# Kernel optimization log

Measured on AMD Instinct MI355X. Metric: run time of the kernel, lower is better.

## Reference

```python
import jax, jax.numpy as jnp
import numpy as np

EPS = 1e-5          # nn.LayerNorm default eps
THRESH = 0.4        # min_entity_score
K = 20              # max_entities_per_text
NUM_TYPES = 8       # len(EntityType) (not in source; fixed constant)


def _mlp(x, w1, b1, g, be, w2, b2):
    """Linear -> LayerNorm -> GELU(exact) -> (Dropout=eval identity) -> Linear."""
    h = x @ w1 + b1
    mu = h.mean(-1, keepdims=True)
    var = ((h - mu) ** 2).mean(-1, keepdims=True)
    h = (h - mu) * jax.lax.rsqrt(var + EPS) * g + be
    h = jax.nn.gelu(h, approximate=False)
    return h @ w2 + b2


def setup_inputs() -> dict:
    key = jax.random.key(0)
    ks = jax.random.split(key, 10)
    B, S, D, H, T = 8, 4096, 1024, 256, NUM_TYPES

    def lin(k, i, o):
        s = 1.0 / np.sqrt(i)
        return jax.random.uniform(k, (i, o), jnp.float32, -s, s)

    return {
        "hidden_states": jax.random.normal(ks[0], (B, S, D), jnp.float32),
        "attention_mask": jax.random.randint(ks[1], (B, S), 0, 2).astype(jnp.int32),
        # entity_scorer params
        "sc_w1": lin(ks[2], D, H), "sc_b1": jnp.zeros((H,), jnp.float32),
        "sc_g": jnp.ones((H,), jnp.float32), "sc_be": jnp.zeros((H,), jnp.float32),
        "sc_w2": lin(ks[3], H, 1), "sc_b2": jnp.zeros((1,), jnp.float32),
        # span_enhancer params
        "en_w1": lin(ks[4], D, H), "en_b1": jnp.zeros((H,), jnp.float32),
        "en_g": jnp.ones((H,), jnp.float32), "en_be": jnp.zeros((H,), jnp.float32),
        "en_w2": lin(ks[5], H, D), "en_b2": jnp.zeros((D,), jnp.float32),
        # type_classifier params
        "ty_w1": lin(ks[6], D, H), "ty_b1": jnp.zeros((H,), jnp.float32),
        "ty_g": jnp.ones((H,), jnp.float32), "ty_be": jnp.zeros((H,), jnp.float32),
        "ty_w2": lin(ks[7], H, T), "ty_b2": jnp.zeros((T,), jnp.float32),
    }


def reference(hidden_states, attention_mask,
              sc_w1, sc_b1, sc_g, sc_be, sc_w2, sc_b2,
              en_w1, en_b1, en_g, en_be, en_w2, en_b2,
              ty_w1, ty_b1, ty_g, ty_be, ty_w2, ty_b2):
    B, S, D = hidden_states.shape
    # per-token entity scores [B, S]
    scores = jax.nn.sigmoid(_mlp(hidden_states, sc_w1, sc_b1, sc_g, sc_be, sc_w2, sc_b2))[..., 0]
    scores = scores * attention_mask.astype(scores.dtype)
    # parallel run-length encoding of spans (replaces serial python loop):
    # a token is inside a span iff score >= thresh and unmasked; spans break on
    # below-threshold or masked tokens, exactly as the serial RLE does.
    above = (scores >= THRESH) & (attention_mask > 0)
    prev = jnp.pad(above[:, :-1], ((0, 0), (1, 0)))
    start = above & ~prev
    sid = jnp.clip(jnp.cumsum(start.astype(jnp.int32), axis=1) - 1, 0)  # span label per token
    seg = (sid + jnp.arange(B, dtype=jnp.int32)[:, None] * S).reshape(-1)
    w = above.astype(scores.dtype)
    nseg = B * S
    span_len = jax.ops.segment_sum(w.reshape(-1), seg, num_segments=nseg).reshape(B, S)
    span_sum = jax.ops.segment_sum((scores * w).reshape(-1), seg, num_segments=nseg).reshape(B, S)
    rep_sum = jax.ops.segment_sum((hidden_states * w[..., None]).reshape(B * S, D), seg,
                                  num_segments=nseg).reshape(B, S, D)
    denom = jnp.maximum(span_len, 1.0)
    avg = span_sum / denom                      # mean token score per span
    valid = (span_len > 0) & (avg >= THRESH)    # avg-score threshold from original
    sel = jnp.where(valid, avg, -1.0)
    # keep at most K highest-scoring spans per batch row (matches global sort + per-batch cap)
    top_vals, top_idx = jax.lax.top_k(sel, K)   # [B, K]
    valid_k = (top_vals >= THRESH).astype(scores.dtype)
    reps = jnp.take_along_axis(rep_sum, top_idx[..., None], axis=1)
    lens = jnp.take_along_axis(denom, top_idx, axis=1)
    reps = reps / lens[..., None] * valid_k[..., None]      # span mean-pooled hidden states
    enhanced = _mlp(reps, en_w1, en_b1, en_g, en_be, en_w2, en_b2) * valid_k[..., None]
    type_logits = _mlp(enhanced, ty_w1, ty_b1, ty_g, ty_be, ty_w2, ty_b2)
    type_probs = jax.nn.softmax(type_logits, axis=-1)
    entity_types = jnp.argmax(type_logits, axis=-1)
    entity_scores = top_vals * valid_k
    return scores, enhanced, type_logits, entity_scores, type_probs, entity_types, valid_k
```

## Files before the change

kernel.cpp:

```cpp
#include <hip/hip_runtime.h>
#include <hip/hip_bf16.h>

#define S_LEN 4096
#define BATCH 8
#define DMODEL 1024
#define HDIM 256
#define NTYPES 8
#define KMAX 20
#define NSLOT (BATCH*KMAX)
#define THRESH 0.4f
#define LN_EPS 1e-5f
#define RSQRT2 0.70710678118654752f

#define O_SCORES 0
#define O_ENH    32768
#define O_TLOG   196608
#define O_ESC    197888
#define O_TPROB  198048
#define O_TYPE   199328
#define O_VALIDK 199488

#define WS_SCORES   0
#define WS_SPSTART  32768
#define WS_SPLEN    49152
#define WS_SPAVG    65536
#define WS_NSP      81920
#define WS_SELSTART 81936
#define WS_SELLEN   82096
#define WS_SELAVG   82256
#define WS_SELVALID 82416
#define WS_IMG      82576

typedef _Float16 f16x8 __attribute__((ext_vector_type(8)));
typedef float f32x16 __attribute__((ext_vector_type(16)));

__device__ __forceinline__ float gelu_exact(float v) {
    return 0.5f * v * (1.0f + erff(v * RSQRT2));
}
__device__ __forceinline__ int kkey(int r) { return (r ^ (r >> 2)) & 3; }

#define GLL16(g, l) __builtin_amdgcn_global_load_lds( \
    (const __attribute__((address_space(1))) unsigned int*)(g), \
    (__attribute__((address_space(3))) unsigned int*)(l), 16, 0, 0)

__global__ __launch_bounds__(256) void k_prep(
    const float* __restrict__ W1, _Float16* __restrict__ IMG)
{
    const int c = blockIdx.x;
    const int n = threadIdx.x;
#pragma unroll
    for (int j = 0; j < 4; j++) {
        f16x8 hv, lv;
#pragma unroll
        for (int e = 0; e < 8; e++) {
            float w = W1[(size_t)(c * 32 + j * 8 + e) * HDIM + n];
            _Float16 h = (_Float16)w;
            hv[e] = h;
            lv[e] = (_Float16)(w - (float)h);
        }
        int off = c * 16384 + n * 32 + ((j ^ kkey(n)) * 8);
        *(f16x8*)&IMG[off] = hv;
        *(f16x8*)&IMG[off + 8192] = lv;
    }
}

__global__ __launch_bounds__(256, 2) void k_score3(
    const float* __restrict__ X, const _Float16* __restrict__ IMG,
    const float* __restrict__ B1, const float* __restrict__ G,
    const float* __restrict__ BE, const float* __restrict__ W2,
    const float* __restrict__ B2, const int* __restrict__ MASK,
    float* __restrict__ scf, float* __restrict__ out)
{
    union SM {
        struct {
            _Float16 A[2][2][2048];
            _Float16 B[2][16384];
        } s;
        struct { float part2[64 * 3]; float mul[64]; float rsl[64]; } e;
    };
    __shared__ SM sm;

    const int tid = threadIdx.x;
    const int lane = tid & 63, wid = tid >> 6;
    const int lr = lane & 31, lh = lane >> 5;
    const int wm = (wid & 1) * 32;
    const int wn = (wid >> 1) * 128;
    const int wg = wid >> 1;
    const int tok0 = blockIdx.x * 64;

    const int arow = tid >> 2, akg = tid & 3;
    const int aoff = arow * 32 + ((akg ^ kkey(arow)) * 8);
    const float* xptr = X + (size_t)(tok0 + arow) * DMODEL + akg * 8;
    const char* gB = (const char*)IMG + wid * 1024 + lane * 16;

    f32x16 acc[4];
#pragma unroll
    for (int ni = 0; ni < 4; ni++) acc[ni] = (f32x16)0.0f;

    {
        float4 xa = *(const float4*)xptr;
        float4 xb = *(const float4*)(xptr + 4);
        char* lB = (char*)sm.s.B[0] + wid * 1024;
#pragma unroll
        for (int r = 0; r < 8; r++) GLL16(gB + r * 4096, lB + r * 4096);
        float xv[8] = {xa.x, xa.y, xa.z, xa.w, xb.x, xb.y, xb.z, xb.w};
        f16x8 ah, al;
#pragma unroll
        for (int e = 0; e < 8; e++) {
            _Float16 h = (_Float16)xv[e];
            ah[e] = h;
            al[e] = (_Float16)(xv[e] - (float)h);
        }
        *(f16x8*)&sm.s.A[0][0][aoff] = ah;
        *(f16x8*)&sm.s.A[0][1][aoff] = al;
    }
    __syncthreads();

    int cur = 0;
    for (int c = 0; c < 32; ++c) {
        float4 nxa, nxb;
        if (c < 31) {
            nxa = *(const float4*)(xptr + (c + 1) * 32);
            nxb = *(const float4*)(xptr + (c + 1) * 32 + 4);
            char* lB = (char*)sm.s.B[cur ^ 1] + wid * 1024;
            const char* g = gB + (size_t)(c + 1) * 32768;
#pragma unroll
            for (int r = 0; r < 8; r++) GLL16(g + r * 4096, lB + r * 4096);
        }
        const _Float16* Ah = sm.s.A[cur][0];
        const _Float16* Al = sm.s.A[cur][1];
        const _Float16* Bc = sm.s.B[cur];
#pragma unroll
        for (int s = 0; s < 2; ++s) {
            const int kg = s * 2 + lh;
            const int row = wm + lr;
            const int oa = row * 32 + ((kg ^ kkey(row)) * 8);
            f16x8 fah = *(const f16x8*)&Ah[oa];
            f16x8 fal = *(const f16x8*)&Al[oa];
#pragma unroll
            for (int ni = 0; ni < 4; ni++) {
                const int col = wn + ni * 32 + lr;
                const int ob = col * 32 + ((kg ^ kkey(col)) * 8);
                f16x8 fbh = *(const f16x8*)&Bc[ob];
                f16x8 fbl = *(const f16x8*)&Bc[8192 + ob];
                acc[ni] = __builtin_amdgcn_mfma_f32_32x32x16_f16(fah, fbh, acc[ni], 0, 0, 0);
                acc[ni] = __builtin_amdgcn_mfma_f32_32x32x16_f16(fal, fbh, acc[ni], 0, 0, 0);
                acc[ni] = __builtin_amdgcn_mfma_f32_32x32x16_f16(fah, fbl, acc[ni], 0, 0, 0);
            }
        }
        if (c < 31) {
            float xv[8] = {nxa.x, nxa.y, nxa.z, nxa.w, nxb.x, nxb.y, nxb.z, nxb.w};
            f16x8 ah, al;
#pragma unroll
            for (int e = 0; e < 8; e++) {
                _Float16 h = (_Float16)xv[e];
                ah[e] = h;
                al[e] = (_Float16)(xv[e] - (float)h);
            }
            *(f16x8*)&sm.s.A[cur ^ 1][0][aoff] = ah;
            *(f16x8*)&sm.s.A[cur ^ 1][1][aoff] = al;
        }
        __syncthreads();
        cur ^= 1;
    }

    float bcol[4], gcol[4], becol[4], wcol[4];
#pragma unroll
    for (int ni = 0; ni < 4; ni++) {
        int colg = wn + ni * 32 + lr;
        bcol[ni] = B1[colg];
        gcol[ni] = G[colg];
        becol[ni] = BE[colg];
        wcol[ni] = W2[colg];
    }
#pragma unroll
    for (int ni = 0; ni < 4; ni++)
#pragma unroll
        for (int r = 0; r < 16; r++) acc[ni][r] += bcol[ni];

#pragma unroll
    for (int r = 0; r < 16; r++) {
        float p = acc[0][r] + acc[1][r] + acc[2][r] + acc[3][r];
        p += __shfl_xor(p, 1);  p += __shfl_xor(p, 2);
        p += __shfl_xor(p, 4);  p += __shfl_xor(p, 8);
        p += __shfl_xor(p, 16);
        int row = wm + (r & 3) + 8 * (r >> 2) + 4 * lh;
        if (lr == 0) sm.e.part2[row * 3 + wg] = p;
    }
    __syncthreads();
    if (tid < 64)
        sm.e.mul[tid] = (sm.e.part2[tid * 3] + sm.e.part2[tid * 3 + 1]) * (1.0f / 256.0f);
    __syncthreads();
#pragma unroll
    for (int r = 0; r < 16; r++) {
        int row = wm + (r & 3) + 8 * (r >> 2) + 4 * lh;
        float m = sm.e.mul[row];
        float p = 0.0f;
#pragma unroll
        for (int ni = 0; ni < 4; ni++) {
            float d = acc[ni][r] - m;
            p += d * d;
        }
        p += __shfl_xor(p, 1);  p += __shfl_xor(p, 2);
        p += __shfl_xor(p, 4);  p += __shfl_xor(p, 8);
        p += __shfl_xor(p, 16);
        if (lr == 0) sm.e.part2[row * 3 + wg] = p;
    }
    __syncthreads();
    if (tid < 64)
        sm.e.rsl[tid] = rsqrtf((sm.e.part2[tid * 3] + sm.e.part2[tid * 3 + 1]) * (1.0f / 256.0f) + LN_EPS);
    __syncthreads();
#pragma unroll
    for (int r = 0; r < 16; r++) {
        int row = wm + (r & 3) + 8 * (r >> 2) + 4 * lh;
        float m = sm.e.mul[row];
        float rv = sm.e.rsl[row];
        float p = 0.0f;
#pragma unroll
        for (int ni = 0; ni < 4; ni++) {
            float v = (acc[ni][r] - m) * rv * gcol[ni] + becol[ni];
            p += gelu_exact(v) * wcol[ni];
        }
        p += __shfl_xor(p, 1);  p += __shfl_xor(p, 2);
        p += __shfl_xor(p, 4);  p += __shfl_xor(p, 8);
        p += __shfl_xor(p, 16);
        if (lr == 0) sm.e.part2[row * 3 + wg] = p;
    }
    __syncthreads();
    if (tid < 64) {
        float s = sm.e.part2[tid * 3] + sm.e.part2[tid * 3 + 1];
        float logit = s + B2[0];
        float sc = 1.0f / (1.0f + expf(-logit));
        int t = tok0 + tid;
        sc *= (float)MASK[t];
        scf[t] = sc;
        out[O_SCORES + t] = sc;
    }
}

__global__ __launch_bounds__(1024) void k_spans(
    const float* __restrict__ scf, int* __restrict__ spstart,
    int* __restrict__ splen, float* __restrict__ spavg, int* __restrict__ nsp,
    int* __restrict__ selstart, int* __restrict__ sellen,
    float* __restrict__ selavg, float* __restrict__ selvalid,
    float* __restrict__ out)
{
    const int r = blockIdx.x, tid = threadIdx.x;
    __shared__ float sc[S_LEN];
    __shared__ unsigned char ab[S_LEN];
    __shared__ int scn[1024];
    __shared__ float avgl[2048];
    __shared__ float rv[16];
    __shared__ int ri[16];

    float4 v = ((const float4*)(scf + (size_t)r * S_LEN))[tid];
    const int s0 = tid * 4;
    sc[s0 + 0] = v.x; sc[s0 + 1] = v.y; sc[s0 + 2] = v.z; sc[s0 + 3] = v.w;
    ab[s0 + 0] = (v.x >= THRESH);
    ab[s0 + 1] = (v.y >= THRESH);
    ab[s0 + 2] = (v.z >= THRESH);
    ab[s0 + 3] = (v.w >= THRESH);
    __syncthreads();

    bool st[4];
    int cnt = 0;
#pragma unroll
    for (int i = 0; i < 4; i++) {
        bool a = ab[s0 + i] != 0;
        bool p = (s0 + i == 0) ? false : (ab[s0 + i - 1] != 0);
        st[i] = a && !p;
        cnt += st[i] ? 1 : 0;
    }
    scn[tid] = cnt;
    __syncthreads();
    for (int off = 1; off < 1024; off <<= 1) {
        int mine = scn[tid];
        int add = (tid >= off) ? scn[tid - off] : 0;
        __syncthreads();
        scn[tid] = mine + add;
        __syncthreads();
    }
    const int total = scn[1023];
    int j = scn[tid] - cnt;
    for (int i = 0; i < 4; i++) {
        if (st[i]) {
            int s = s0 + i;
            float sum = 0.0f;
            int len = 0;
            int e = s;
            while (e < S_LEN && ab[e]) { sum += sc[e]; len++; e++; }
            float avg = sum / (float)len;
            spstart[r * 2048 + j] = s;
            splen[r * 2048 + j] = len;
            spavg[r * 2048 + j] = avg;
            avgl[j] = avg;
            j++;
        }
    }
    if (tid == 0) nsp[r] = total;
    __syncthreads();

    for (int k = 0; k < KMAX; k++) {
        float bv = -3.0e38f;
        int bi = 0x7FFFFFFF;
        for (int q = tid; q < total; q += 1024) {
            float a = avgl[q];
            if (a > bv) { bv = a; bi = q; }
        }
#pragma unroll
        for (int m = 1; m < 64; m <<= 1) {
            float ov = __shfl_xor(bv, m);
            int oi = __shfl_xor(bi, m);
            if (ov > bv || (ov == bv && oi < bi)) { bv = ov; bi = oi; }
        }
        if ((tid & 63) == 0) { rv[tid >> 6] = bv; ri[tid >> 6] = bi; }
        __syncthreads();
        if (tid < 64) {
            float v2 = (tid < 16) ? rv[tid] : -3.0e38f;
            int i2 = (tid < 16) ? ri[tid] : 0x7FFFFFFF;
#pragma unroll
            for (int m = 1; m < 16; m <<= 1) {
                float ov = __shfl_xor(v2, m);
                int oi = __shfl_xor(i2, m);
                if (ov > v2 || (ov == v2 && oi < i2)) { v2 = ov; i2 = oi; }
            }
            if (tid == 0) {
                int slot = r * KMAX + k;
                if (k < total) {
                    avgl[i2] = -3.0e38f;
                    int ln = splen[r * 2048 + i2];
                    float vd = (v2 >= THRESH && ln > 0) ? 1.0f : 0.0f;
                    selstart[slot] = spstart[r * 2048 + i2];
                    sellen[slot] = ln;
                    selavg[slot] = v2;
                    selvalid[slot] = vd;
                    out[O_ESC + slot] = v2 * vd;
                    out[O_VALIDK + slot] = vd;
                } else {
                    selstart[slot] = -1;
                    sellen[slot] = 0;
                    selavg[slot] = -1.0f;
                    selvalid[slot] = 0.0f;
                    out[O_ESC + slot] = 0.0f;
                    out[O_VALIDK + slot] = 0.0f;
                }
            }
        }
        __syncthreads();
    }
}

__global__ __launch_bounds__(1024) void k_tail2(
    const float* __restrict__ X, const int* __restrict__ selstart,
    const int* __restrict__ sellen, const float* __restrict__ selvalid,
    const float* __restrict__ en_w1, const float* __restrict__ en_b1,
    const float* __restrict__ en_g, const float* __restrict__ en_be,
    const float* __restrict__ en_w2, const float* __restrict__ en_b2,
    const float* __restrict__ ty_w1, const float* __restrict__ ty_b1,
    const float* __restrict__ ty_g, const float* __restrict__ ty_be,
    const float* __restrict__ ty_w2, const float* __restrict__ ty_b2,
    float* __restrict__ out)
{
    const int slot = blockIdx.x, tid = threadIdx.x;
    __shared__ float xr[DMODEL];
    __shared__ float ps[DMODEL];
    __shared__ float g1[HDIM];
    __shared__ float red[8];
    __shared__ float lgp[4 * NTYPES];
    __shared__ float lg[NTYPES];

    const int r = slot / KMAX;
    const int s0 = selstart[slot], ln = sellen[slot];
    const float vd = selvalid[slot];
    const int j = tid & 255, p = tid >> 8;

    {
        float a = 0.0f;
        if (s0 >= 0) {
            const float* base = X + ((size_t)r * S_LEN + s0) * DMODEL + tid;
#pragma unroll 4
            for (int t = 0; t < ln; t++) a += base[(size_t)t * DMODEL];
        }
        const float dn = (ln > 0) ? (float)ln : 1.0f;
        xr[tid] = a / dn * vd;
    }
    __syncthreads();

    {
        float acc = 0.0f;
        const float* wp = en_w1 + (size_t)(p * 256) * HDIM + j;
        const float* xp = xr + p * 256;
#pragma unroll 16
        for (int k = 0; k < 256; k++) acc += xp[k] * wp[(size_t)k * HDIM];
        ps[tid] = acc;
    }
    __syncthreads();
    float h = 0.0f, mu = 0.0f;
    if (tid < 256) {
        h = ps[tid] + ps[256 + tid] + ps[512 + tid] + ps[768 + tid] + en_b1[tid];
        float s = h;
#pragma unroll
        for (int m = 1; m < 64; m <<= 1) s += __shfl_xor(s, m);
        if ((tid & 63) == 0) red[tid >> 6] = s;
    }
    __syncthreads();
    if (tid < 256) {
        mu = (red[0] + red[1] + red[2] + red[3]) * (1.0f / 256.0f);
        float d = h - mu;
        float s = d * d;
#pragma unroll
        for (int m = 1; m < 64; m <<= 1) s += __shfl_xor(s, m);
        if ((tid & 63) == 0) red[4 + (tid >> 6)] = s;
    }
    __syncthreads();
    if (tid < 256) {
        float var = (red[4] + red[5] + red[6] + red[7]) * (1.0f / 256.0f);
        float v = (h - mu) * rsqrtf(var + LN_EPS) * en_g[tid] + en_be[tid];
        g1[tid] = gelu_exact(v);
    }
    __syncthreads();

    {
        float acc = en_b2[tid];
        const float* wp = en_w2 + tid;
#pragma unroll 16
        for (int k = 0; k < 256; k++) acc += g1[k] * wp[(size_t)k * DMODEL];
        acc *= vd;
        out[O_ENH + (size_t)slot * DMODEL + tid] = acc;
        xr[tid] = acc;
    }
    __syncthreads();

    {
        float acc = 0.0f;
        const float* wp = ty_w1 + (size_t)(p * 256) * HDIM + j;
        const float* xp = xr + p * 256;
#pragma unroll 16
        for (int k = 0; k < 256; k++) acc += xp[k] * wp[(size_t)k * HDIM];
        ps[tid] = acc;
    }
    __syncthreads();
    h = 0.0f; mu = 0.0f;
    if (tid < 256) {
        h = ps[tid] + ps[256 + tid] + ps[512 + tid] + ps[768 + tid] + ty_b1[tid];
        float s = h;
#pragma unroll
        for (int m = 1; m < 64; m <<= 1) s += __shfl_xor(s, m);
        if ((tid & 63) == 0) red[tid >> 6] = s;
    }
    __syncthreads();
    if (tid < 256) {
        mu = (red[0] + red[1] + red[2] + red[3]) * (1.0f / 256.0f);
        float d = h - mu;
        float s = d * d;
#pragma unroll
        for (int m = 1; m < 64; m <<= 1) s += __shfl_xor(s, m);
        if ((tid & 63) == 0) red[4 + (tid >> 6)] = s;
    }
    __syncthreads();
    if (tid < 256) {
        float var = (red[4] + red[5] + red[6] + red[7]) * (1.0f / 256.0f);
        float v = (h - mu) * rsqrtf(var + LN_EPS) * ty_g[tid] + ty_be[tid];
        g1[tid] = gelu_exact(v);
    }
    __syncthreads();

    if (tid < 256) {
        float gv = g1[tid];
        float4 w0 = *(const float4*)&ty_w2[tid * NTYPES];
        float4 w1v = *(const float4*)&ty_w2[tid * NTYPES + 4];
        float pj[8] = {gv * w0.x, gv * w0.y, gv * w0.z, gv * w0.w,
                       gv * w1v.x, gv * w1v.y, gv * w1v.z, gv * w1v.w};
#pragma unroll
        for (int q = 0; q < 8; q++) {
            float s = pj[q];
#pragma unroll
            for (int m = 1; m < 64; m <<= 1) s += __shfl_xor(s, m);
            pj[q] = s;
        }
        if ((tid & 63) == 0) {
#pragma unroll
            for (int q = 0; q < 8; q++) lgp[(tid >> 6) * NTYPES + q] = pj[q];
        }
    }
    __syncthreads();
    if (tid < NTYPES) {
        float la = ty_b2[tid] + lgp[tid] + lgp[NTYPES + tid] +
                   lgp[2 * NTYPES + tid] + lgp[3 * NTYPES + tid];
        lg[tid] = la;
        out[O_TLOG + slot * NTYPES + tid] = la;
    }
    __syncthreads();
    if (tid == 0) {
        float mx = lg[0];
        int am = 0;
        for (int t = 1; t < NTYPES; t++)
            if (lg[t] > mx) { mx = lg[t]; am = t; }
        float ex[NTYPES], ssum = 0.0f;
        for (int t = 0; t < NTYPES; t++) { ex[t] = expf(lg[t] - mx); ssum += ex[t]; }
        for (int t = 0; t < NTYPES; t++)
            out[O_TPROB + slot * NTYPES + t] = ex[t] / ssum;
        out[O_TYPE + slot] = (float)am;
    }
}

extern "C" void kernel_launch(void* const* d_in, const int* in_sizes, int n_in,
                              void* d_out, int out_size, void* d_ws, size_t ws_size,
                              hipStream_t stream) {
    const float* X = (const float*)d_in[0];
    const int* MASK = (const int*)d_in[1];
    const float* sc_w1 = (const float*)d_in[2];
    const float* sc_b1 = (const float*)d_in[3];
    const float* sc_g  = (const float*)d_in[4];
    const float* sc_be = (const float*)d_in[5];
    const float* sc_w2 = (const float*)d_in[6];
    const float* sc_b2 = (const float*)d_in[7];
    const float* en_w1 = (const float*)d_in[8];
    const float* en_b1 = (const float*)d_in[9];
    const float* en_g  = (const float*)d_in[10];
    const float* en_be = (const float*)d_in[11];
    const float* en_w2 = (const float*)d_in[12];
    const float* en_b2 = (const float*)d_in[13];
    const float* ty_w1 = (const float*)d_in[14];
    const float* ty_b1 = (const float*)d_in[15];
    const float* ty_g  = (const float*)d_in[16];
    const float* ty_be = (const float*)d_in[17];
    const float* ty_w2 = (const float*)d_in[18];
    const float* ty_b2 = (const float*)d_in[19];

    float* out = (float*)d_out;
    float* wsf = (float*)d_ws;
    int* wsi = (int*)d_ws;
    _Float16* img = (_Float16*)(wsf + WS_IMG);

    k_prep<<<32, 256, 0, stream>>>(sc_w1, img);
    k_score3<<<(BATCH * S_LEN) / 64, 256, 0, stream>>>(
        X, img, sc_b1, sc_g, sc_be, sc_w2, sc_b2, MASK, wsf + WS_SCORES, out);
    k_spans<<<BATCH, 1024, 0, stream>>>(
        wsf + WS_SCORES, wsi + WS_SPSTART, wsi + WS_SPLEN, wsf + WS_SPAVG,
        wsi + WS_NSP, wsi + WS_SELSTART, wsi + WS_SELLEN, wsf + WS_SELAVG,
        wsf + WS_SELVALID, out);
    k_tail2<<<NSLOT, 1024, 0, stream>>>(
        X, wsi + WS_SELSTART, wsi + WS_SELLEN, wsf + WS_SELVALID,
        en_w1, en_b1, en_g, en_be, en_w2, en_b2,
        ty_w1, ty_b1, ty_g, ty_be, ty_w2, ty_b2, out);
}
```

Before: 155.7 us.

## Double the scorer token tile and triple-buffer weight loads with explicit waitcnt barriers

The scoring GEMM kernel now processes 128 tokens per block with 512 threads (8 waves), so each B-weight tile staged in LDS is reused across twice as many rows. B tiles move from a double buffer to a triple buffer prefetched two chunks ahead, and __syncthreads is replaced by a partial vmcnt wait plus s_barrier so outstanding async loads can stay in flight across iterations. The aim is to halve weight-tile traffic per token and hide global-load latency. In exchange, LDS use per block rises and the wrap-around prefetches in the final iterations perform redundant loads.

```diff
diff --git a/kernel.cpp b/kernel.cpp
--- a/kernel.cpp
+++ b/kernel.cpp
@@ -64,7 +64,7 @@
     }
 }
 
-__global__ __launch_bounds__(256, 2) void k_score3(
+__global__ __launch_bounds__(512, 2) void k_score4(
     const float* __restrict__ X, const _Float16* __restrict__ IMG,
     const float* __restrict__ B1, const float* __restrict__ G,
     const float* __restrict__ BE, const float* __restrict__ W2,
@@ -73,25 +73,25 @@
 {
     union SM {
         struct {
-            _Float16 A[2][2][2048];
-            _Float16 B[2][16384];
+            _Float16 A[2][2][4096];
+            _Float16 B[3][16384];
         } s;
-        struct { float part2[64 * 3]; float mul[64]; float rsl[64]; } e;
+        struct { float part2[128 * 3]; float mul[128]; float rsl[128]; } e;
     };
     __shared__ SM sm;
 
     const int tid = threadIdx.x;
     const int lane = tid & 63, wid = tid >> 6;
     const int lr = lane & 31, lh = lane >> 5;
-    const int wm = (wid & 1) * 32;
-    const int wn = (wid >> 1) * 128;
-    const int wg = wid >> 1;
-    const int tok0 = blockIdx.x * 64;
+    const int wm = (wid & 3) * 32;
+    const int wn = (wid >> 2) * 128;
+    const int wg = wid >> 2;
+    const int tok0 = blockIdx.x * 128;
 
     const int arow = tid >> 2, akg = tid & 3;
     const int aoff = arow * 32 + ((akg ^ kkey(arow)) * 8);
     const float* xptr = X + (size_t)(tok0 + arow) * DMODEL + akg * 8;
-    const char* gB = (const char*)IMG + wid * 1024 + lane * 16;
+    const char* gB = (const char*)IMG + wid * 4096 + lane * 16;
 
     f32x16 acc[4];
 #pragma unroll
@@ -100,9 +100,12 @@
     {
         float4 xa = *(const float4*)xptr;
         float4 xb = *(const float4*)(xptr + 4);
-        char* lB = (char*)sm.s.B[0] + wid * 1024;
-#pragma unroll
-        for (int r = 0; r < 8; r++) GLL16(gB + r * 4096, lB + r * 4096);
+        char* lB0 = (char*)sm.s.B[0] + wid * 4096;
+        char* lB1 = (char*)sm.s.B[1] + wid * 4096;
+#pragma unroll
+        for (int r = 0; r < 4; r++) GLL16(gB + r * 1024, lB0 + r * 1024);
+#pragma unroll
+        for (int r = 0; r < 4; r++) GLL16(gB + 32768 + r * 1024, lB1 + r * 1024);
         float xv[8] = {xa.x, xa.y, xa.z, xa.w, xb.x, xb.y, xb.z, xb.w};
         f16x8 ah, al;
 #pragma unroll
@@ -114,41 +117,48 @@
         *(f16x8*)&sm.s.A[0][0][aoff] = ah;
         *(f16x8*)&sm.s.A[0][1][aoff] = al;
     }
-    __syncthreads();
-
-    int cur = 0;
+    asm volatile("s_waitcnt vmcnt(4) lgkmcnt(0)" ::: "memory");
+    __builtin_amdgcn_s_barrier();
+    __builtin_amdgcn_sched_barrier(0);
+
+    int bc = 0;
+    int ac = 0;
     for (int c = 0; c < 32; ++c) {
-        float4 nxa, nxb;
-        if (c < 31) {
-            nxa = *(const float4*)(xptr + (c + 1) * 32);
-            nxb = *(const float4*)(xptr + (c + 1) * 32 + 4);
-            char* lB = (char*)sm.s.B[cur ^ 1] + wid * 1024;
-            const char* g = gB + (size_t)(c + 1) * 32768;
-#pragma unroll
-            for (int r = 0; r < 8; r++) GLL16(g + r * 4096, lB + r * 4096);
-        }
-        const _Float16* Ah = sm.s.A[cur][0];
-        const _Float16* Al = sm.s.A[cur][1];
-        const _Float16* Bc = sm.s.B[cur];
-#pragma unroll
-        for (int s = 0; s < 2; ++s) {
-            const int kg = s * 2 + lh;
-            const int row = wm + lr;
-            const int oa = row * 32 + ((kg ^ kkey(row)) * 8);
-            f16x8 fah = *(const f16x8*)&Ah[oa];
-            f16x8 fal = *(const f16x8*)&Al[oa];
-#pragma unroll
-            for (int ni = 0; ni < 4; ni++) {
-                const int col = wn + ni * 32 + lr;
-                const int ob = col * 32 + ((kg ^ kkey(col)) * 8);
-                f16x8 fbh = *(const f16x8*)&Bc[ob];
-                f16x8 fbl = *(const f16x8*)&Bc[8192 + ob];
-                acc[ni] = __builtin_amdgcn_mfma_f32_32x32x16_f16(fah, fbh, acc[ni], 0, 0, 0);
-                acc[ni] = __builtin_amdgcn_mfma_f32_32x32x16_f16(fal, fbh, acc[ni], 0, 0, 0);
-                acc[ni] = __builtin_amdgcn_mfma_f32_32x32x16_f16(fah, fbl, acc[ni], 0, 0, 0);
+        const int cn = (c + 1) & 31;
+        const int c2 = (c + 2) & 31;
+        int b2 = bc - 1; if (b2 < 0) b2 = 2;
+        float4 nxa = *(const float4*)(xptr + cn * 32);
+        float4 nxb = *(const float4*)(xptr + cn * 32 + 4);
+        {
+            char* lB = (char*)sm.s.B[b2] + wid * 4096;
+            const char* g = (const char*)IMG + (size_t)c2 * 32768 + wid * 4096 + lane * 16;
+#pragma unroll
+            for (int r = 0; r < 4; r++) GLL16(g + r * 1024, lB + r * 1024);
+        }
+        {
+            const _Float16* Ah = sm.s.A[ac][0];
+            const _Float16* Al = sm.s.A[ac][1];
+            const _Float16* Bc = sm.s.B[bc];
+#pragma unroll
+            for (int s = 0; s < 2; ++s) {
+                const int kg = s * 2 + lh;
+                const int row = wm + lr;
+                const int oa = row * 32 + ((kg ^ kkey(row)) * 8);
+                f16x8 fah = *(const f16x8*)&Ah[oa];
+                f16x8 fal = *(const f16x8*)&Al[oa];
+#pragma unroll
+                for (int ni = 0; ni < 4; ni++) {
+                    const int col = wn + ni * 32 + lr;
+                    const int ob = col * 32 + ((kg ^ kkey(col)) * 8);
+                    f16x8 fbh = *(const f16x8*)&Bc[ob];
+                    f16x8 fbl = *(const f16x8*)&Bc[8192 + ob];
+                    acc[ni] = __builtin_amdgcn_mfma_f32_32x32x16_f16(fah, fbh, acc[ni], 0, 0, 0);
+                    acc[ni] = __builtin_amdgcn_mfma_f32_32x32x16_f16(fal, fbh, acc[ni], 0, 0, 0);
+                    acc[ni] = __builtin_amdgcn_mfma_f32_32x32x16_f16(fah, fbl, acc[ni], 0, 0, 0);
+                }
             }
         }
-        if (c < 31) {
+        {
             float xv[8] = {nxa.x, nxa.y, nxa.z, nxa.w, nxb.x, nxb.y, nxb.z, nxb.w};
             f16x8 ah, al;
 #pragma unroll
@@ -157,12 +167,17 @@
                 ah[e] = h;
                 al[e] = (_Float16)(xv[e] - (float)h);
             }
-            *(f16x8*)&sm.s.A[cur ^ 1][0][aoff] = ah;
-            *(f16x8*)&sm.s.A[cur ^ 1][1][aoff] = al;
-        }
-        __syncthreads();
-        cur ^= 1;
-    }
+            *(f16x8*)&sm.s.A[ac ^ 1][0][aoff] = ah;
+            *(f16x8*)&sm.s.A[ac ^ 1][1][aoff] = al;
+        }
+        asm volatile("s_waitcnt vmcnt(4) lgkmcnt(0)" ::: "memory");
+        __builtin_amdgcn_s_barrier();
+        __builtin_amdgcn_sched_barrier(0);
+        bc = bc == 2 ? 0 : bc + 1;
+        ac ^= 1;
+    }
+
+    __syncthreads();
 
     float bcol[4], gcol[4], becol[4], wcol[4];
 #pragma unroll
@@ -188,7 +203,7 @@
         if (lr == 0) sm.e.part2[row * 3 + wg] = p;
     }
     __syncthreads();
-    if (tid < 64)
+    if (tid < 128)
         sm.e.mul[tid] = (sm.e.part2[tid * 3] + sm.e.part2[tid * 3 + 1]) * (1.0f / 256.0f);
     __syncthreads();
 #pragma unroll
@@ -207,7 +222,7 @@
         if (lr == 0) sm.e.part2[row * 3 + wg] = p;
     }
     __syncthreads();
-    if (tid < 64)
+    if (tid < 128)
         sm.e.rsl[tid] = rsqrtf((sm.e.part2[tid * 3] + sm.e.part2[tid * 3 + 1]) * (1.0f / 256.0f) + LN_EPS);
     __syncthreads();
 #pragma unroll
@@ -227,7 +242,7 @@
         if (lr == 0) sm.e.part2[row * 3 + wg] = p;
     }
     __syncthreads();
-    if (tid < 64) {
+    if (tid < 128) {
         float s = sm.e.part2[tid * 3] + sm.e.part2[tid * 3 + 1];
         float logit = s + B2[0];
         float sc = 1.0f / (1.0f + expf(-logit));
@@ -534,7 +549,7 @@
     _Float16* img = (_Float16*)(wsf + WS_IMG);
 
     k_prep<<<32, 256, 0, stream>>>(sc_w1, img);
-    k_score3<<<(BATCH * S_LEN) / 64, 256, 0, stream>>>(
+    k_score4<<<(BATCH * S_LEN) / 128, 512, 0, stream>>>(
         X, img, sc_b1, sc_g, sc_be, sc_w2, sc_b2, MASK, wsf + WS_SCORES, out);
     k_spans<<<BATCH, 1024, 0, stream>>>(
         wsf + WS_SCORES, wsi + WS_SPSTART, wsi + WS_SPLEN, wsf + WS_SPAVG,
```

New measurement: 154.6 us. No clear change (-0.7%).

## Load W1 fragments directly to registers and widen score kernel to 512 threads

Applied to the files above, without the earlier changes.

The scoring GEMM kernel no longer stages the fp16 hi/lo W1 image through LDS with global_load_lds. Each wave now reads its B fragments straight from global memory (L2-resident) into registers, prefetched two K-steps ahead, and only the split X tile goes through a small double-buffered LDS. The block grows to 8 waves each covering 64 columns, the K step shrinks to 16, the prep kernel writes a matching unswizzled layout, and the epilogue reductions sum four partials per row. This cuts LDS footprint and traffic to raise occupancy, but doubles the number of barriers per tile and relies on cache hits for repeated W1 reads.

```diff
diff --git a/kernel.cpp b/kernel.cpp
--- a/kernel.cpp
+++ b/kernel.cpp
@@ -31,40 +31,37 @@
 #define WS_SELVALID 82416
 #define WS_IMG      82576
 
+typedef _Float16 f16x2 __attribute__((ext_vector_type(2)));
 typedef _Float16 f16x8 __attribute__((ext_vector_type(8)));
 typedef float f32x16 __attribute__((ext_vector_type(16)));
 
 __device__ __forceinline__ float gelu_exact(float v) {
     return 0.5f * v * (1.0f + erff(v * RSQRT2));
 }
-__device__ __forceinline__ int kkey(int r) { return (r ^ (r >> 2)) & 3; }
-
-#define GLL16(g, l) __builtin_amdgcn_global_load_lds( \
-    (const __attribute__((address_space(1))) unsigned int*)(g), \
-    (__attribute__((address_space(3))) unsigned int*)(l), 16, 0, 0)
 
 __global__ __launch_bounds__(256) void k_prep(
     const float* __restrict__ W1, _Float16* __restrict__ IMG)
 {
     const int c = blockIdx.x;
     const int n = threadIdx.x;
-#pragma unroll
-    for (int j = 0; j < 4; j++) {
-        f16x8 hv, lv;
+    f16x8 hv[2], lv[2];
+#pragma unroll
+    for (int j = 0; j < 2; j++)
 #pragma unroll
         for (int e = 0; e < 8; e++) {
-            float w = W1[(size_t)(c * 32 + j * 8 + e) * HDIM + n];
+            float w = W1[(size_t)(c * 16 + j * 8 + e) * HDIM + n];
             _Float16 h = (_Float16)w;
-            hv[e] = h;
-            lv[e] = (_Float16)(w - (float)h);
-        }
-        int off = c * 16384 + n * 32 + ((j ^ kkey(n)) * 8);
-        *(f16x8*)&IMG[off] = hv;
-        *(f16x8*)&IMG[off + 8192] = lv;
-    }
+            hv[j][e] = h;
+            lv[j][e] = (_Float16)(w - (float)h);
+        }
+    const int off = c * 8192 + n * 16;
+    *(f16x8*)&IMG[off] = hv[0];
+    *(f16x8*)&IMG[off + 8] = hv[1];
+    *(f16x8*)&IMG[off + 4096] = lv[0];
+    *(f16x8*)&IMG[off + 4096 + 8] = lv[1];
 }
 
-__global__ __launch_bounds__(256, 2) void k_score3(
+__global__ __launch_bounds__(512, 4) void k_score6(
     const float* __restrict__ X, const _Float16* __restrict__ IMG,
     const float* __restrict__ B1, const float* __restrict__ G,
     const float* __restrict__ BE, const float* __restrict__ W2,
@@ -72,11 +69,8 @@
     float* __restrict__ scf, float* __restrict__ out)
 {
     union SM {
-        struct {
-            _Float16 A[2][2][2048];
-            _Float16 B[2][16384];
-        } s;
-        struct { float part2[64 * 3]; float mul[64]; float rsl[64]; } e;
+        _Float16 A[2][2][1024];
+        struct { float part2[64 * 5]; float mul[64]; float rsl[64]; } e;
     };
     __shared__ SM sm;
 
@@ -84,89 +78,83 @@
     const int lane = tid & 63, wid = tid >> 6;
     const int lr = lane & 31, lh = lane >> 5;
     const int wm = (wid & 1) * 32;
-    const int wn = (wid >> 1) * 128;
-    const int wg = wid >> 1;
+    const int wn = (wid >> 1) * 64;
+    const int wnid = wid >> 1;
     const int tok0 = blockIdx.x * 64;
 
-    const int arow = tid >> 2, akg = tid & 3;
-    const int aoff = arow * 32 + ((akg ^ kkey(arow)) * 8);
-    const float* xptr = X + (size_t)(tok0 + arow) * DMODEL + akg * 8;
-    const char* gB = (const char*)IMG + wid * 1024 + lane * 16;
-
-    f32x16 acc[4];
-#pragma unroll
-    for (int ni = 0; ni < 4; ni++) acc[ni] = (f32x16)0.0f;
-
+    const int xrow = tid >> 3, xk = (tid & 7) * 2;
+    const float* xbase = X + (size_t)(tok0 + xrow) * DMODEL + xk;
+    const int awoff = xrow * 16 + xk;
+    const int aroff = (wm + lr) * 16 + lh * 8;
+    const int bo0 = (wn + lr) * 16 + lh * 8;
+    const int bo1 = (wn + 32 + lr) * 16 + lh * 8;
+
+    f32x16 acc0 = (f32x16)0.0f, acc1 = (f32x16)0.0f;
+
+    float2 x0 = *(const float2*)xbase;
+    f16x8 bh0c = *(const f16x8*)&IMG[bo0];
+    f16x8 bh1c = *(const f16x8*)&IMG[bo1];
+    f16x8 bl0c = *(const f16x8*)&IMG[4096 + bo0];
+    f16x8 bl1c = *(const f16x8*)&IMG[4096 + bo1];
     {
-        float4 xa = *(const float4*)xptr;
-        float4 xb = *(const float4*)(xptr + 4);
-        char* lB = (char*)sm.s.B[0] + wid * 1024;
-#pragma unroll
-        for (int r = 0; r < 8; r++) GLL16(gB + r * 4096, lB + r * 4096);
-        float xv[8] = {xa.x, xa.y, xa.z, xa.w, xb.x, xb.y, xb.z, xb.w};
-        f16x8 ah, al;
-#pragma unroll
-        for (int e = 0; e < 8; e++) {
-            _Float16 h = (_Float16)xv[e];
-            ah[e] = h;
-            al[e] = (_Float16)(xv[e] - (float)h);
-        }
-        *(f16x8*)&sm.s.A[0][0][aoff] = ah;
-        *(f16x8*)&sm.s.A[0][1][aoff] = al;
-    }
-    __syncthreads();
+        _Float16 h0 = (_Float16)x0.x, h1 = (_Float16)x0.y;
+        f16x2 hh = {h0, h1};
+        f16x2 ll = {(_Float16)(x0.x - (float)h0), (_Float16)(x0.y - (float)h1)};
+        *(f16x2*)&sm.A[0][0][awoff] = hh;
+        *(f16x2*)&sm.A[0][1][awoff] = ll;
+    }
+    float2 xnext = *(const float2*)(xbase + 16);
+    f16x8 bh0n = *(const f16x8*)&IMG[8192 + bo0];
+    f16x8 bh1n = *(const f16x8*)&IMG[8192 + bo1];
+    f16x8 bl0n = *(const f16x8*)&IMG[8192 + 4096 + bo0];
+    f16x8 bl1n = *(const f16x8*)&IMG[8192 + 4096 + bo1];
+    asm volatile("s_waitcnt lgkmcnt(0)" ::: "memory");
+    __builtin_amdgcn_s_barrier();
+    __builtin_amdgcn_sched_barrier(0);
 
     int cur = 0;
-    for (int c = 0; c < 32; ++c) {
-        float4 nxa, nxb;
-        if (c < 31) {
-            nxa = *(const float4*)(xptr + (c + 1) * 32);
-            nxb = *(const float4*)(xptr + (c + 1) * 32 + 4);
-            char* lB = (char*)sm.s.B[cur ^ 1] + wid * 1024;
-            const char* g = gB + (size_t)(c + 1) * 32768;
-#pragma unroll
-            for (int r = 0; r < 8; r++) GLL16(g + r * 4096, lB + r * 4096);
-        }
-        const _Float16* Ah = sm.s.A[cur][0];
-        const _Float16* Al = sm.s.A[cur][1];
-        const _Float16* Bc = sm.s.B[cur];
-#pragma unroll
-        for (int s = 0; s < 2; ++s) {
-            const int kg = s * 2 + lh;
-            const int row = wm + lr;
-            const int oa = row * 32 + ((kg ^ kkey(row)) * 8);
-            f16x8 fah = *(const f16x8*)&Ah[oa];
-            f16x8 fal = *(const f16x8*)&Al[oa];
-#pragma unroll
-            for (int ni = 0; ni < 4; ni++) {
-                const int col = wn + ni * 32 + lr;
-                const int ob = col * 32 + ((kg ^ kkey(col)) * 8);
-                f16x8 fbh = *(const f16x8*)&Bc[ob];
-                f16x8 fbl = *(const f16x8*)&Bc[8192 + ob];
-                acc[ni] = __builtin_amdgcn_mfma_f32_32x32x16_f16(fah, fbh, acc[ni], 0, 0, 0);
-                acc[ni] = __builtin_amdgcn_mfma_f32_32x32x16_f16(fal, fbh, acc[ni], 0, 0, 0);
-                acc[ni] = __builtin_amdgcn_mfma_f32_32x32x16_f16(fah, fbl, acc[ni], 0, 0, 0);
-            }
-        }
-        if (c < 31) {
-            float xv[8] = {nxa.x, nxa.y, nxa.z, nxa.w, nxb.x, nxb.y, nxb.z, nxb.w};
-            f16x8 ah, al;
-#pragma unroll
-            for (int e = 0; e < 8; e++) {
-                _Float16 h = (_Float16)xv[e];
-                ah[e] = h;
-                al[e] = (_Float16)(xv[e] - (float)h);
-            }
-            *(f16x8*)&sm.s.A[cur ^ 1][0][aoff] = ah;
-            *(f16x8*)&sm.s.A[cur ^ 1][1][aoff] = al;
-        }
-        __syncthreads();
+#pragma unroll 2
+    for (int c = 0; c < 64; ++c) {
+        const int cf = (c + 2) & 63;
+        float2 xfut = *(const float2*)(xbase + cf * 16);
+        const _Float16* ib = IMG + cf * 8192;
+        f16x8 fbh0 = *(const f16x8*)&ib[bo0];
+        f16x8 fbh1 = *(const f16x8*)&ib[bo1];
+        f16x8 fbl0 = *(const f16x8*)&ib[4096 + bo0];
+        f16x8 fbl1 = *(const f16x8*)&ib[4096 + bo1];
+
+        f16x8 fah = *(const f16x8*)&sm.A[cur][0][aroff];
+        f16x8 fal = *(const f16x8*)&sm.A[cur][1][aroff];
+
+        acc0 = __builtin_amdgcn_mfma_f32_32x32x16_f16(fah, bh0c, acc0, 0, 0, 0);
+        acc0 = __builtin_amdgcn_mfma_f32_32x32x16_f16(fal, bh0c, acc0, 0, 0, 0);
+        acc0 = __builtin_amdgcn_mfma_f32_32x32x16_f16(fah, bl0c, acc0, 0, 0, 0);
+        acc1 = __builtin_amdgcn_mfma_f32_32x32x16_f16(fah, bh1c, acc1, 0, 0, 0);
+        acc1 = __builtin_amdgcn_mfma_f32_32x32x16_f16(fal, bh1c, acc1, 0, 0, 0);
+        acc1 = __builtin_amdgcn_mfma_f32_32x32x16_f16(fah, bl1c, acc1, 0, 0, 0);
+
+        {
+            _Float16 h0 = (_Float16)xnext.x, h1 = (_Float16)xnext.y;
+            f16x2 hh = {h0, h1};
+            f16x2 ll = {(_Float16)(xnext.x - (float)h0), (_Float16)(xnext.y - (float)h1)};
+            *(f16x2*)&sm.A[cur ^ 1][0][awoff] = hh;
+            *(f16x2*)&sm.A[cur ^ 1][1][awoff] = ll;
+        }
+        asm volatile("s_waitcnt lgkmcnt(0)" ::: "memory");
+        __builtin_amdgcn_s_barrier();
+        __builtin_amdgcn_sched_barrier(0);
+
+        bh0c = bh0n; bh1c = bh1n; bl0c = bl0n; bl1c = bl1n;
+        bh0n = fbh0; bh1n = fbh1; bl0n = fbl0; bl1n = fbl1;
+        xnext = xfut;
         cur ^= 1;
     }
 
-    float bcol[4], gcol[4], becol[4], wcol[4];
-#pragma unroll
-    for (int ni = 0; ni < 4; ni++) {
+    __syncthreads();
+
+    float bcol[2], gcol[2], becol[2], wcol[2];
+#pragma unroll
+    for (int ni = 0; ni < 2; ni++) {
         int colg = wn + ni * 32 + lr;
         bcol[ni] = B1[colg];
         gcol[ni] = G[colg];
@@ -174,61 +162,55 @@
         wcol[ni] = W2[colg];
     }
 #pragma unroll
-    for (int ni = 0; ni < 4; ni++)
-#pragma unroll
-        for (int r = 0; r < 16; r++) acc[ni][r] += bcol[ni];
+    for (int r = 0; r < 16; r++) { acc0[r] += bcol[0]; acc1[r] += bcol[1]; }
 
 #pragma unroll
     for (int r = 0; r < 16; r++) {
-        float p = acc[0][r] + acc[1][r] + acc[2][r] + acc[3][r];
+        float p = acc0[r] + acc1[r];
         p += __shfl_xor(p, 1);  p += __shfl_xor(p, 2);
         p += __shfl_xor(p, 4);  p += __shfl_xor(p, 8);
         p += __shfl_xor(p, 16);
         int row = wm + (r & 3) + 8 * (r >> 2) + 4 * lh;
-        if (lr == 0) sm.e.part2[row * 3 + wg] = p;
+        if (lr == 0) sm.e.part2[row * 5 + wnid] = p;
     }
     __syncthreads();
     if (tid < 64)
-        sm.e.mul[tid] = (sm.e.part2[tid * 3] + sm.e.part2[tid * 3 + 1]) * (1.0f / 256.0f);
+        sm.e.mul[tid] = (sm.e.part2[tid * 5] + sm.e.part2[tid * 5 + 1] +
+                         sm.e.part2[tid * 5 + 2] + sm.e.part2[tid * 5 + 3]) * (1.0f / 256.0f);
     __syncthreads();
 #pragma unroll
     for (int r = 0; r < 16; r++) {
         int row = wm + (r & 3) + 8 * (r >> 2) + 4 * lh;
         float m = sm.e.mul[row];
-        float p = 0.0f;
-#pragma unroll
-        for (int ni = 0; ni < 4; ni++) {
-            float d = acc[ni][r] - m;
-            p += d * d;
-        }
+        float d0 = acc0[r] - m, d1 = acc1[r] - m;
+        float p = d0 * d0 + d1 * d1;
         p += __shfl_xor(p, 1);  p += __shfl_xor(p, 2);
         p += __shfl_xor(p, 4);  p += __shfl_xor(p, 8);
         p += __shfl_xor(p, 16);
-        if (lr == 0) sm.e.part2[row * 3 + wg] = p;
+        if (lr == 0) sm.e.part2[row * 5 + wnid] = p;
     }
     __syncthreads();
     if (tid < 64)
-        sm.e.rsl[tid] = rsqrtf((sm.e.part2[tid * 3] + sm.e.part2[tid * 3 + 1]) * (1.0f / 256.0f) + LN_EPS);
+        sm.e.rsl[tid] = rsqrtf((sm.e.part2[tid * 5] + sm.e.part2[tid * 5 + 1] +
+                                sm.e.part2[tid * 5 + 2] + sm.e.part2[tid * 5 + 3]) * (1.0f / 256.0f) + LN_EPS);
     __syncthreads();
 #pragma unroll
     for (int r = 0; r < 16; r++) {
         int row = wm + (r & 3) + 8 * (r >> 2) + 4 * lh;
         float m = sm.e.mul[row];
         float rv = sm.e.rsl[row];
-        float p = 0.0f;
-#pragma unroll
-        for (int ni = 0; ni < 4; ni++) {
-            float v = (acc[ni][r] - m) * rv * gcol[ni] + becol[ni];
-            p += gelu_exact(v) * wcol[ni];
-        }
+        float v0 = (acc0[r] - m) * rv * gcol[0] + becol[0];
+        float v1 = (acc1[r] - m) * rv * gcol[1] + becol[1];
+        float p = gelu_exact(v0) * wcol[0] + gelu_exact(v1) * wcol[1];
         p += __shfl_xor(p, 1);  p += __shfl_xor(p, 2);
         p += __shfl_xor(p, 4);  p += __shfl_xor(p, 8);
         p += __shfl_xor(p, 16);
-        if (lr == 0) sm.e.part2[row * 3 + wg] = p;
+        if (lr == 0) sm.e.part2[row * 5 + wnid] = p;
     }
     __syncthreads();
     if (tid < 64) {
-        float s = sm.e.part2[tid * 3] + sm.e.part2[tid * 3 + 1];
+        float s = sm.e.part2[tid * 5] + sm.e.part2[tid * 5 + 1] +
+                  sm.e.part2[tid * 5 + 2] + sm.e.part2[tid * 5 + 3];
         float logit = s + B2[0];
         float sc = 1.0f / (1.0f + expf(-logit));
         int t = tok0 + tid;
@@ -533,8 +515,8 @@
     int* wsi = (int*)d_ws;
     _Float16* img = (_Float16*)(wsf + WS_IMG);
 
-    k_prep<<<32, 256, 0, stream>>>(sc_w1, img);
-    k_score3<<<(BATCH * S_LEN) / 64, 256, 0, stream>>>(
+    k_prep<<<64, 256, 0, stream>>>(sc_w1, img);
+    k_score6<<<(BATCH * S_LEN) / 64, 512, 0, stream>>>(
         X, img, sc_b1, sc_g, sc_be, sc_w2, sc_b2, MASK, wsf + WS_SCORES, out);
     k_spans<<<BATCH, 1024, 0, stream>>>(
         wsf + WS_SCORES, wsi + WS_SPSTART, wsi + WS_SPLEN, wsf + WS_SPAVG,
```

Result: slower. 164.1 us (+5.4%).
